# Kernel tuning notes

Measured on AMD Instinct MI355X. Metric: run time of the kernel, lower is better.

Reference implementation:

```python
import jax, jax.numpy as jnp
import numpy as np

B, T, K = 512, 1024, 64


def setup_inputs() -> dict:
    key = jax.random.key(0)
    k1, k2, k3, k4, k5 = jax.random.split(key, 5)
    emissions = jax.random.normal(k1, (B, T, K), dtype=jnp.float32)
    tags = jax.random.randint(k2, (B, T), 0, K, dtype=jnp.int64)
    mask = jnp.ones((B, T), dtype=bool)
    transitions = jax.random.uniform(k3, (K, K), minval=-0.1, maxval=0.1, dtype=jnp.float32)
    start_transitions = jax.random.uniform(k4, (K,), minval=-0.1, maxval=0.1, dtype=jnp.float32)
    end_transitions = jax.random.uniform(k5, (K,), minval=-0.1, maxval=0.1, dtype=jnp.float32)
    return {
        "emissions": emissions,
        "transitions": transitions,
        "start_transitions": start_transitions,
        "end_transitions": end_transitions,
        "tags": tags,
        "mask": mask,
    }


def _compute_score(emissions, transitions, start_transitions, end_transitions, tags, mask):
    # emissions: (B,T,K), tags: (B,T), mask: (B,T) bool
    maskf = mask.astype(emissions.dtype)
    # emission scores at gold tags, all positions: (B,T)
    emit = jnp.take_along_axis(emissions, tags[:, :, None], axis=2)[:, :, 0]
    score = emit[:, 0] + start_transitions[tags[:, 0]]
    # transition scores between consecutive gold tags: (B,T-1)
    trans = transitions[tags[:, :-1], tags[:, 1:]]
    score = score + jnp.sum((emit[:, 1:] + trans) * maskf[:, 1:], axis=1)
    seq_lengths = jnp.sum(mask.astype(jnp.int32), axis=1) - 1  # (B,)
    last_tags = jnp.take_along_axis(tags, seq_lengths[:, None], axis=1)[:, 0]
    score = score + end_transitions[last_tags]
    return score


def _log_partition(emissions, transitions, start_transitions, end_transitions, mask):
    maskf = mask.astype(emissions.dtype)
    alpha0 = emissions[:, 0] + start_transitions[None, :]  # (B,K)

    def step(alpha, xs):
        emit_t, mask_t = xs  # (B,K), (B,)
        # inner: (B, K_prev, K_cur)
        inner = alpha[:, :, None] + transitions[None, :, :] + emit_t[:, None, :]
        new_alpha = jax.nn.logsumexp(inner, axis=1)
        m = mask_t[:, None]
        alpha = new_alpha * m + alpha * (1.0 - m)
        return alpha, None

    xs = (jnp.swapaxes(emissions[:, 1:], 0, 1), jnp.swapaxes(maskf[:, 1:], 0, 1))
    alpha, _ = jax.lax.scan(step, alpha0, xs)
    alpha = alpha + end_transitions[None, :]
    return jax.nn.logsumexp(alpha, axis=1)  # (B,)


def reference(emissions, transitions, start_transitions, end_transitions, tags, mask):
    numerator = _compute_score(emissions, transitions, start_transitions, end_transitions, tags, mask)
    denominator = _log_partition(emissions, transitions, start_transitions, end_transitions, mask)
    return jnp.mean(denominator - numerator)
```

## Files before the change

### kernel.cpp

```cpp
#include <hip/hip_runtime.h>


#define CRF_B 512
#define CRF_T 1024
#define CRF_K 64

typedef float f32x2 __attribute__((ext_vector_type(2)));

#define SWZF(v, imm) \
  __int_as_float(__builtin_amdgcn_ds_swizzle(__float_as_int(v), (imm)))

#define DPPF(v, ctrl)                                                      \
  __int_as_float(__builtin_amdgcn_mov_dpp(__float_as_int(v), (ctrl), 0xF,  \
                                          0xF, true))
#define CTL_X1 0xB1
#define CTL_X2 0x4E
#define CTL_X3 0x1B
#define CTL_MIR 0x140
#define CTL_HMIR 0x141

__device__ __forceinline__ float red_add16(float x) {
  auto r = __builtin_amdgcn_permlane16_swap(__float_as_int(x),
                                            __float_as_int(x), false, false);
  return __int_as_float(r[0]) + __int_as_float(r[1]);
}
__device__ __forceinline__ float red_add32(float x) {
  auto r = __builtin_amdgcn_permlane32_swap(__float_as_int(x),
                                            __float_as_int(x), false, false);
  return __int_as_float(r[0]) + __int_as_float(r[1]);
}

#define SP2(x) ((f32x2){(x), (x)})
#define PFMA(b, k, acc) __builtin_elementwise_fma(SP2(b), (k), (acc))

#define PIN_P()                                                            \
  asm volatile("" : "+v"(kp0), "+v"(kp1), "+v"(kp2), "+v"(kp3), "+v"(kp4), \
                    "+v"(kp5), "+v"(kp6), "+v"(kp7), "+v"(kp8), "+v"(kp9), \
                    "+v"(kp10), "+v"(kp11), "+v"(kp12), "+v"(kp13),        \
                    "+v"(kp14), "+v"(kp15))
#define PIN_R()                                                            \
  asm volatile("" : "+v"(kr0), "+v"(kr1), "+v"(kr2), "+v"(kr3), "+v"(kr4), \
                    "+v"(kr5), "+v"(kr6), "+v"(kr7), "+v"(kr8), "+v"(kr9), \
                    "+v"(kr10), "+v"(kr11), "+v"(kr12), "+v"(kr13),        \
                    "+v"(kr14), "+v"(kr15))

#define GLOAD4(buf, ptr)                                                   \
  asm volatile("global_load_dword %0, %4, off\n\t"                         \
               "global_load_dword %1, %4, off offset:256\n\t"              \
               "global_load_dword %2, %4, off offset:512\n\t"              \
               "global_load_dword %3, %4, off offset:768"                  \
               : "=v"(buf[0]), "=v"(buf[1]), "=v"(buf[2]), "=v"(buf[3])    \
               : "v"(ptr))

#define WAITN(n)                                                           \
  do {                                                                     \
    asm volatile("s_waitcnt vmcnt(" #n ")" ::: "memory");                  \
    __builtin_amdgcn_sched_barrier(0);                                     \
  } while (0)

#define STEP(EV, APPLY, DOMAX)                                             \
  do {                                                                     \
    float t1 = DPPF(sv, CTL_X1), t2 = DPPF(sv, CTL_X2);                    \
    float t3 = DPPF(sv, CTL_X3);                                           \
    float t7 = DPPF(sv, CTL_HMIR), tF = DPPF(sv, CTL_MIR);                 \
    float t4 = DPPF(t7, CTL_X3), t5 = DPPF(t7, CTL_X2);                    \
    float t6 = DPPF(t7, CTL_X1), t8 = DPPF(t7, CTL_MIR);                   \
    float tC = DPPF(tF, CTL_X3), tD = DPPF(tF, CTL_X2);                    \
    float tE = DPPF(tF, CTL_X1);                                           \
    float t9 = DPPF(t8, CTL_X1), tA = DPPF(t8, CTL_X2);                    \
    float tB = DPPF(t8, CTL_X3);                                           \
    float xe = __expf(EV);                                                 \
    if (APPLY) xe = ldexpf(xe, -exs);                                      \
    f32x2 accP = SP2(sv) * kp0, accR = SP2(sv) * kr0;                      \
    f32x2 accQ = SP2(t1) * kp1, accS = SP2(t1) * kr1;                      \
    accP = PFMA(t2, kp2, accP);   accR = PFMA(t2, kr2, accR);              \
    accQ = PFMA(t3, kp3, accQ);   accS = PFMA(t3, kr3, accS);              \
    accP = PFMA(t4, kp4, accP);   accR = PFMA(t4, kr4, accR);              \
    accQ = PFMA(t5, kp5, accQ);   accS = PFMA(t5, kr5, accS);              \
    accP = PFMA(t6, kp6, accP);   accR = PFMA(t6, kr6, accR);              \
    accQ = PFMA(t7, kp7, accQ);   accS = PFMA(t7, kr7, accS);              \
    accP = PFMA(t8, kp8, accP);   accR = PFMA(t8, kr8, accR);              \
    accQ = PFMA(t9, kp9, accQ);   accS = PFMA(t9, kr9, accS);              \
    accP = PFMA(tA, kp10, accP);  accR = PFMA(tA, kr10, accR);             \
    accQ = PFMA(tB, kp11, accQ);  accS = PFMA(tB, kr11, accS);             \
    accP = PFMA(tC, kp12, accP);  accR = PFMA(tC, kr12, accR);             \
    accQ = PFMA(tD, kp13, accQ);  accS = PFMA(tD, kr13, accS);             \
    accP = PFMA(tE, kp14, accP);  accR = PFMA(tE, kr14, accR);             \
    accQ = PFMA(tF, kp15, accQ);  accS = PFMA(tF, kr15, accS);             \
    f32x2 a01 = accP + accQ;                                               \
    f32x2 a23 = accR + accS;                                               \
    auto eA = __builtin_amdgcn_permlane32_swap(                            \
        __float_as_int(a01.x), __float_as_int(a23.x), false, false);       \
    float sE = __int_as_float(eA[0]) + __int_as_float(eA[1]);              \
    auto oA = __builtin_amdgcn_permlane32_swap(                            \
        __float_as_int(a01.y), __float_as_int(a23.y), false, false);       \
    float sO = __int_as_float(oA[0]) + __int_as_float(oA[1]);              \
    auto fB = __builtin_amdgcn_permlane16_swap(                            \
        __float_as_int(sE), __float_as_int(sO), false, false);             \
    float red = __int_as_float(fB[0]) + __int_as_float(fB[1]);             \
    sv = red * xe;                                                         \
    if (DOMAX) {                                                           \
      int exl;                                                             \
      (void)frexpf(sv, &exl);                                              \
      exs = __builtin_amdgcn_readfirstlane(exl);                           \
      cexp += exs;                                                         \
    }                                                                      \
  } while (0)

__global__ void __attribute__((amdgpu_flat_work_group_size(64, 64)))
__attribute__((amdgpu_waves_per_eu(1, 1))) crf_fused_kernel(
    const float* __restrict__ emissions, const float* __restrict__ transitions,
    const float* __restrict__ start_t, const float* __restrict__ end_t,
    const int* __restrict__ tags32, float* __restrict__ d_out) {
  const int l = threadIdx.x;
  const int q = l >> 4;
  const int r = l & 15;
  const int b = blockIdx.x;

  f32x2 kp0, kp1, kp2, kp3, kp4, kp5, kp6, kp7;
  f32x2 kp8, kp9, kp10, kp11, kp12, kp13, kp14, kp15;
  f32x2 kr0, kr1, kr2, kr3, kr4, kr5, kr6, kr7;
  f32x2 kr8, kr9, kr10, kr11, kr12, kr13, kr14, kr15;
#define LK(pv, rv, m)                                                  \
  do {                                                                 \
    const float* row = transitions + (16 * q + (r ^ (m))) * CRF_K + r; \
    pv = (f32x2){__expf(row[0]), __expf(row[16])};                     \
    rv = (f32x2){__expf(row[32]), __expf(row[48])};                    \
  } while (0)
  LK(kp0, kr0, 0);   LK(kp1, kr1, 1);   LK(kp2, kr2, 2);
  LK(kp3, kr3, 3);   LK(kp4, kr4, 4);   LK(kp5, kr5, 5);
  LK(kp6, kr6, 6);   LK(kp7, kr7, 7);   LK(kp8, kr8, 8);
  LK(kp9, kr9, 9);   LK(kp10, kr10, 10); LK(kp11, kr11, 11);
  LK(kp12, kr12, 12); LK(kp13, kr13, 13); LK(kp14, kr14, 14);
  LK(kp15, kr15, 15);
#undef LK
  PIN_P();
  PIN_R();

  const float* eptr = emissions + (size_t)b * (CRF_T * CRF_K) + l;

  float sv = __expf(eptr[0] + start_t[l]);
  int exs, cexp = 0;
  {
    int exl;
    (void)frexpf(sv, &exl);
    exs = __builtin_amdgcn_readfirstlane(exl);
    cexp += exs;
  }

  float ea[4], eb[4], ec[4];
  const float* p = eptr + CRF_K;
  GLOAD4(ea, p);
  p += 4 * CRF_K;
  GLOAD4(eb, p);
  p += 4 * CRF_K;

  for (int gg = 0; gg < 84; ++gg) {
    PIN_P();
    PIN_R();
    GLOAD4(ec, p);
    p += 4 * CRF_K;
    WAITN(8);
    STEP(ea[0], true, false);
    STEP(ea[1], false, false);
    STEP(ea[2], false, false);
    STEP(ea[3], false, true);
    GLOAD4(ea, p);
    p += 4 * CRF_K;
    WAITN(8);
    STEP(eb[0], true, false);
    STEP(eb[1], false, false);
    STEP(eb[2], false, false);
    STEP(eb[3], false, true);
    GLOAD4(eb, p);
    p += 4 * CRF_K;
    WAITN(8);
    STEP(ec[0], true, false);
    STEP(ec[1], false, false);
    STEP(ec[2], false, false);
    STEP(ec[3], false, true);
  }

  float ecl[4], eal[3];
#pragma unroll
  for (int k = 0; k < 4; ++k) ecl[k] = eptr[(size_t)(1017 + k) * CRF_K];
#pragma unroll
  for (int k = 0; k < 3; ++k) eal[k] = eptr[(size_t)(1021 + k) * CRF_K];
  WAITN(11);
  STEP(ea[0], true, false);
  STEP(ea[1], false, false);
  STEP(ea[2], false, false);
  STEP(ea[3], false, true);
  WAITN(7);
  STEP(eb[0], true, false);
  STEP(eb[1], false, false);
  STEP(eb[2], false, false);
  STEP(eb[3], false, true);
  STEP(ecl[0], true, false);
  STEP(ecl[1], false, false);
  STEP(ecl[2], false, false);
  STEP(ecl[3], false, true);
  STEP(eal[0], true, false);
  STEP(eal[1], false, false);
  STEP(eal[2], false, false);

  float v = sv * __expf(end_t[l]);
  v += SWZF(v, 0x041F);
  v += SWZF(v, 0x081F);
  v += SWZF(v, 0x101F);
  v += SWZF(v, 0x201F);
  v = red_add32(red_add16(v));
  const float logZ = (float)cexp * 0.69314718055994530942f + logf(v);

  int hv = tags32[2 * l + 1];
  unsigned long long any = __ballot(hv != 0);
  const int mult = (any == 0ULL) ? 2 : 1;
  const size_t tbase = (size_t)b * CRF_T;
  const float* ebase = emissions + (size_t)b * (CRF_T * CRF_K);

  float sacc = 0.f;
#pragma unroll
  for (int it = 0; it < 16; ++it) {
    const int t = l + 64 * it;
    const int tg = tags32[(tbase + (size_t)t) * (size_t)mult];
    float c = ebase[(size_t)t * CRF_K + tg];
    if (t == 0)
      c += start_t[tg];
    else
      c += transitions[tags32[(tbase + (size_t)t - 1) * (size_t)mult] * CRF_K +
                       tg];
    if (t == CRF_T - 1) c += end_t[tg];
    sacc += c;
  }
  sacc += SWZF(sacc, 0x041F);
  sacc += SWZF(sacc, 0x081F);
  sacc += SWZF(sacc, 0x101F);
  sacc += SWZF(sacc, 0x201F);
  sacc = red_add32(red_add16(sacc));

  if (l == 0) d_out[b] = logZ - sacc;
}

__global__ __launch_bounds__(512) void crf_final_kernel(
    const float* __restrict__ d, float* __restrict__ out) {
  const int tid = threadIdx.x;
  float v = d[tid];
#pragma unroll
  for (int off = 32; off >= 1; off >>= 1) v += __shfl_xor(v, off, 64);
  __shared__ float red[8];
  if ((tid & 63) == 0) red[tid >> 6] = v;
  __syncthreads();
  if (tid == 0) {
    float s = 0.f;
#pragma unroll
    for (int i = 0; i < 8; ++i) s += red[i];
    out[0] = s * (1.0f / CRF_B);
  }
}

extern "C" void kernel_launch(void* const* d_in, const int* in_sizes, int n_in,
                              void* d_out, int out_size, void* d_ws,
                              size_t ws_size, hipStream_t stream) {
  const float* emissions   = (const float*)d_in[0];
  const float* transitions = (const float*)d_in[1];
  const float* start_t     = (const float*)d_in[2];
  const float* end_t       = (const float*)d_in[3];
  const int*   tags        = (const int*)d_in[4];

  float* out = (float*)d_out;
  float* d   = (float*)d_ws;

  crf_fused_kernel<<<CRF_B, 64, 0, stream>>>(emissions, transitions, start_t,
                                             end_t, tags, d);
  crf_final_kernel<<<1, 512, 0, stream>>>(d, out);
}
```

Baseline: 303.4 us.

## Process two batch rows per wavefront with interleaved forward recurrences

Each 64-lane block now runs the forward recurrence for two sequences at once, interleaving two independent dependency chains so their latencies can hide each other. The grid is halved to 256 blocks, and the transition matrix held in registers is shared by both chains. The cost is more registers and emission loads per wave, and with only 256 blocks on a GPU that has more CUs than that, some CUs may sit idle. The serial chain per block also becomes longer.

```diff
diff --git a/kernel.cpp b/kernel.cpp
--- a/kernel.cpp
+++ b/kernel.cpp
@@ -58,7 +58,7 @@
     __builtin_amdgcn_sched_barrier(0);                                     \
   } while (0)
 
-#define STEP(EV, APPLY, DOMAX)                                             \
+#define STEPC(sv, exs, cexp, EV, APPLY, DOMAX)                             \
   do {                                                                     \
     float t1 = DPPF(sv, CTL_X1), t2 = DPPF(sv, CTL_X2);                    \
     float t3 = DPPF(sv, CTL_X3);                                           \
@@ -107,6 +107,12 @@
     }                                                                      \
   } while (0)
 
+#define STEP2(EVA, EVB, APPLY, DOMAX)                                      \
+  do {                                                                     \
+    STEPC(svA, exsA, cexpA, EVA, APPLY, DOMAX);                            \
+    STEPC(svB, exsB, cexpB, EVB, APPLY, DOMAX);                            \
+  } while (0)
+
 __global__ void __attribute__((amdgpu_flat_work_group_size(64, 64)))
 __attribute__((amdgpu_waves_per_eu(1, 1))) crf_fused_kernel(
     const float* __restrict__ emissions, const float* __restrict__ transitions,
@@ -115,7 +121,8 @@
   const int l = threadIdx.x;
   const int q = l >> 4;
   const int r = l & 15;
-  const int b = blockIdx.x;
+  const int b0 = 2 * blockIdx.x;
+  const int b1 = b0 + 1;
 
   f32x2 kp0, kp1, kp2, kp3, kp4, kp5, kp6, kp7;
   f32x2 kp8, kp9, kp10, kp11, kp12, kp13, kp14, kp15;
@@ -137,108 +144,150 @@
   PIN_P();
   PIN_R();
 
-  const float* eptr = emissions + (size_t)b * (CRF_T * CRF_K) + l;
-
-  float sv = __expf(eptr[0] + start_t[l]);
-  int exs, cexp = 0;
+  const float* eptrA = emissions + (size_t)b0 * (CRF_T * CRF_K) + l;
+  const float* eptrB = emissions + (size_t)b1 * (CRF_T * CRF_K) + l;
+
+  float svA = __expf(eptrA[0] + start_t[l]);
+  float svB = __expf(eptrB[0] + start_t[l]);
+  int exsA, exsB, cexpA = 0, cexpB = 0;
   {
     int exl;
-    (void)frexpf(sv, &exl);
-    exs = __builtin_amdgcn_readfirstlane(exl);
-    cexp += exs;
-  }
-
-  float ea[4], eb[4], ec[4];
-  const float* p = eptr + CRF_K;
-  GLOAD4(ea, p);
-  p += 4 * CRF_K;
-  GLOAD4(eb, p);
-  p += 4 * CRF_K;
+    (void)frexpf(svA, &exl);
+    exsA = __builtin_amdgcn_readfirstlane(exl);
+    cexpA += exsA;
+    (void)frexpf(svB, &exl);
+    exsB = __builtin_amdgcn_readfirstlane(exl);
+    cexpB += exsB;
+  }
+
+  float eaA[4], ebA[4], ecA[4], eaB[4], ebB[4], ecB[4];
+  const float* pA = eptrA + CRF_K;
+  const float* pB = eptrB + CRF_K;
+  GLOAD4(eaA, pA);
+  GLOAD4(eaB, pB);
+  pA += 4 * CRF_K;
+  pB += 4 * CRF_K;
+  GLOAD4(ebA, pA);
+  GLOAD4(ebB, pB);
+  pA += 4 * CRF_K;
+  pB += 4 * CRF_K;
 
   for (int gg = 0; gg < 84; ++gg) {
     PIN_P();
     PIN_R();
-    GLOAD4(ec, p);
-    p += 4 * CRF_K;
-    WAITN(8);
-    STEP(ea[0], true, false);
-    STEP(ea[1], false, false);
-    STEP(ea[2], false, false);
-    STEP(ea[3], false, true);
-    GLOAD4(ea, p);
-    p += 4 * CRF_K;
-    WAITN(8);
-    STEP(eb[0], true, false);
-    STEP(eb[1], false, false);
-    STEP(eb[2], false, false);
-    STEP(eb[3], false, true);
-    GLOAD4(eb, p);
-    p += 4 * CRF_K;
-    WAITN(8);
-    STEP(ec[0], true, false);
-    STEP(ec[1], false, false);
-    STEP(ec[2], false, false);
-    STEP(ec[3], false, true);
-  }
-
-  float ecl[4], eal[3];
-#pragma unroll
-  for (int k = 0; k < 4; ++k) ecl[k] = eptr[(size_t)(1017 + k) * CRF_K];
-#pragma unroll
-  for (int k = 0; k < 3; ++k) eal[k] = eptr[(size_t)(1021 + k) * CRF_K];
-  WAITN(11);
-  STEP(ea[0], true, false);
-  STEP(ea[1], false, false);
-  STEP(ea[2], false, false);
-  STEP(ea[3], false, true);
-  WAITN(7);
-  STEP(eb[0], true, false);
-  STEP(eb[1], false, false);
-  STEP(eb[2], false, false);
-  STEP(eb[3], false, true);
-  STEP(ecl[0], true, false);
-  STEP(ecl[1], false, false);
-  STEP(ecl[2], false, false);
-  STEP(ecl[3], false, true);
-  STEP(eal[0], true, false);
-  STEP(eal[1], false, false);
-  STEP(eal[2], false, false);
-
-  float v = sv * __expf(end_t[l]);
-  v += SWZF(v, 0x041F);
-  v += SWZF(v, 0x081F);
-  v += SWZF(v, 0x101F);
-  v += SWZF(v, 0x201F);
-  v = red_add32(red_add16(v));
-  const float logZ = (float)cexp * 0.69314718055994530942f + logf(v);
+    GLOAD4(ecA, pA);
+    GLOAD4(ecB, pB);
+    pA += 4 * CRF_K;
+    pB += 4 * CRF_K;
+    WAITN(16);
+    STEP2(eaA[0], eaB[0], true, false);
+    STEP2(eaA[1], eaB[1], false, false);
+    STEP2(eaA[2], eaB[2], false, false);
+    STEP2(eaA[3], eaB[3], false, true);
+    GLOAD4(eaA, pA);
+    GLOAD4(eaB, pB);
+    pA += 4 * CRF_K;
+    pB += 4 * CRF_K;
+    WAITN(16);
+    STEP2(ebA[0], ebB[0], true, false);
+    STEP2(ebA[1], ebB[1], false, false);
+    STEP2(ebA[2], ebB[2], false, false);
+    STEP2(ebA[3], ebB[3], false, true);
+    GLOAD4(ebA, pA);
+    GLOAD4(ebB, pB);
+    pA += 4 * CRF_K;
+    pB += 4 * CRF_K;
+    WAITN(16);
+    STEP2(ecA[0], ecB[0], true, false);
+    STEP2(ecA[1], ecB[1], false, false);
+    STEP2(ecA[2], ecB[2], false, false);
+    STEP2(ecA[3], ecB[3], false, true);
+  }
+
+  float eclA[4], ealA[3], eclB[4], ealB[3];
+#pragma unroll
+  for (int k = 0; k < 4; ++k) {
+    eclA[k] = eptrA[(size_t)(1017 + k) * CRF_K];
+    eclB[k] = eptrB[(size_t)(1017 + k) * CRF_K];
+  }
+#pragma unroll
+  for (int k = 0; k < 3; ++k) {
+    ealA[k] = eptrA[(size_t)(1021 + k) * CRF_K];
+    ealB[k] = eptrB[(size_t)(1021 + k) * CRF_K];
+  }
+  WAITN(0);
+  STEP2(eaA[0], eaB[0], true, false);
+  STEP2(eaA[1], eaB[1], false, false);
+  STEP2(eaA[2], eaB[2], false, false);
+  STEP2(eaA[3], eaB[3], false, true);
+  STEP2(ebA[0], ebB[0], true, false);
+  STEP2(ebA[1], ebB[1], false, false);
+  STEP2(ebA[2], ebB[2], false, false);
+  STEP2(ebA[3], ebB[3], false, true);
+  STEP2(eclA[0], eclB[0], true, false);
+  STEP2(eclA[1], eclB[1], false, false);
+  STEP2(eclA[2], eclB[2], false, false);
+  STEP2(eclA[3], eclB[3], false, true);
+  STEP2(ealA[0], ealB[0], true, false);
+  STEP2(ealA[1], ealB[1], false, false);
+  STEP2(ealA[2], ealB[2], false, false);
+
+  float ee = __expf(end_t[l]);
+  float logZA, logZB;
+  {
+    float v = svA * ee;
+    v += SWZF(v, 0x041F);
+    v += SWZF(v, 0x081F);
+    v += SWZF(v, 0x101F);
+    v += SWZF(v, 0x201F);
+    v = red_add32(red_add16(v));
+    logZA = (float)cexpA * 0.69314718055994530942f + logf(v);
+  }
+  {
+    float v = svB * ee;
+    v += SWZF(v, 0x041F);
+    v += SWZF(v, 0x081F);
+    v += SWZF(v, 0x101F);
+    v += SWZF(v, 0x201F);
+    v = red_add32(red_add16(v));
+    logZB = (float)cexpB * 0.69314718055994530942f + logf(v);
+  }
 
   int hv = tags32[2 * l + 1];
   unsigned long long any = __ballot(hv != 0);
   const int mult = (any == 0ULL) ? 2 : 1;
-  const size_t tbase = (size_t)b * CRF_T;
-  const float* ebase = emissions + (size_t)b * (CRF_T * CRF_K);
-
-  float sacc = 0.f;
-#pragma unroll
-  for (int it = 0; it < 16; ++it) {
-    const int t = l + 64 * it;
-    const int tg = tags32[(tbase + (size_t)t) * (size_t)mult];
-    float c = ebase[(size_t)t * CRF_K + tg];
-    if (t == 0)
-      c += start_t[tg];
-    else
-      c += transitions[tags32[(tbase + (size_t)t - 1) * (size_t)mult] * CRF_K +
-                       tg];
-    if (t == CRF_T - 1) c += end_t[tg];
-    sacc += c;
-  }
-  sacc += SWZF(sacc, 0x041F);
-  sacc += SWZF(sacc, 0x081F);
-  sacc += SWZF(sacc, 0x101F);
-  sacc += SWZF(sacc, 0x201F);
-  sacc = red_add32(red_add16(sacc));
-
-  if (l == 0) d_out[b] = logZ - sacc;
+
+  float sc[2];
+#pragma unroll
+  for (int c = 0; c < 2; ++c) {
+    const size_t tbase = (size_t)(b0 + c) * CRF_T;
+    const float* ebase = emissions + (size_t)(b0 + c) * (CRF_T * CRF_K);
+    float sacc = 0.f;
+#pragma unroll
+    for (int it = 0; it < 16; ++it) {
+      const int t = l + 64 * it;
+      const int tg = tags32[(tbase + (size_t)t) * (size_t)mult];
+      float cv = ebase[(size_t)t * CRF_K + tg];
+      if (t == 0)
+        cv += start_t[tg];
+      else
+        cv += transitions[tags32[(tbase + (size_t)t - 1) * (size_t)mult] *
+                              CRF_K + tg];
+      if (t == CRF_T - 1) cv += end_t[tg];
+      sacc += cv;
+    }
+    sacc += SWZF(sacc, 0x041F);
+    sacc += SWZF(sacc, 0x081F);
+    sacc += SWZF(sacc, 0x101F);
+    sacc += SWZF(sacc, 0x201F);
+    sacc = red_add32(red_add16(sacc));
+    sc[c] = sacc;
+  }
+
+  if (l == 0) {
+    d_out[b0] = logZA - sc[0];
+    d_out[b1] = logZB - sc[1];
+  }
 }
 
 __global__ __launch_bounds__(512) void crf_final_kernel(
@@ -270,7 +319,7 @@
   float* out = (float*)d_out;
   float* d   = (float*)d_ws;
 
-  crf_fused_kernel<<<CRF_B, 64, 0, stream>>>(emissions, transitions, start_t,
-                                             end_t, tags, d);
+  crf_fused_kernel<<<CRF_B / 2, 64, 0, stream>>>(emissions, transitions,
+                                                 start_t, end_t, tags, d);
   crf_final_kernel<<<1, 512, 0, stream>>>(d, out);
 }
```

New measurement: 437.4 us. 44.2% more time.

## Restructure CRF forward step to per-lane output with cross-row shuffles instead of permlane reductions

Applied to the files above, without the earlier changes.

Each lane now computes its full output column directly. Three xor-shuffles broadcast the other 16-lane row groups of alpha, DPP permutations run within each group, and a scalar FMA chain with register-resident exp(transitions) follows. This removes the packed f32x2 FMAs and the permlane32/16 swap reduction tree at the end of each step. The cost is 64 scalar FMAs per step instead of 32 packed ones, plus __shfl_xor calls, which may lower to ds_bpermute through LDS and add latency on the serial recurrence.

```diff
diff --git a/kernel.cpp b/kernel.cpp
--- a/kernel.cpp
+++ b/kernel.cpp
@@ -5,7 +5,7 @@
 #define CRF_T 1024
 #define CRF_K 64
 
-typedef float f32x2 __attribute__((ext_vector_type(2)));
+typedef float f32x4 __attribute__((ext_vector_type(4)));
 
 #define SWZF(v, imm) \
   __int_as_float(__builtin_amdgcn_ds_swizzle(__float_as_int(v), (imm)))
@@ -30,19 +30,11 @@
   return __int_as_float(r[0]) + __int_as_float(r[1]);
 }
 
-#define SP2(x) ((f32x2){(x), (x)})
-#define PFMA(b, k, acc) __builtin_elementwise_fma(SP2(b), (k), (acc))
-
-#define PIN_P()                                                            \
-  asm volatile("" : "+v"(kp0), "+v"(kp1), "+v"(kp2), "+v"(kp3), "+v"(kp4), \
-                    "+v"(kp5), "+v"(kp6), "+v"(kp7), "+v"(kp8), "+v"(kp9), \
-                    "+v"(kp10), "+v"(kp11), "+v"(kp12), "+v"(kp13),        \
-                    "+v"(kp14), "+v"(kp15))
-#define PIN_R()                                                            \
-  asm volatile("" : "+v"(kr0), "+v"(kr1), "+v"(kr2), "+v"(kr3), "+v"(kr4), \
-                    "+v"(kr5), "+v"(kr6), "+v"(kr7), "+v"(kr8), "+v"(kr9), \
-                    "+v"(kr10), "+v"(kr11), "+v"(kr12), "+v"(kr13),        \
-                    "+v"(kr14), "+v"(kr15))
+#define PIN_K()                                                            \
+  asm volatile("" : "+v"(k0_0), "+v"(k0_1), "+v"(k0_2), "+v"(k0_3),        \
+                    "+v"(k1_0), "+v"(k1_1), "+v"(k1_2), "+v"(k1_3),        \
+                    "+v"(k2_0), "+v"(k2_1), "+v"(k2_2), "+v"(k2_3),        \
+                    "+v"(k3_0), "+v"(k3_1), "+v"(k3_2), "+v"(k3_3))
 
 #define GLOAD4(buf, ptr)                                                   \
   asm volatile("global_load_dword %0, %4, off\n\t"                         \
@@ -58,46 +50,42 @@
     __builtin_amdgcn_sched_barrier(0);                                     \
   } while (0)
 
+#define GROUP(S, aE, aO, kv0, kv1, kv2, kv3)                               \
+  {                                                                        \
+    float t7 = DPPF(S, CTL_HMIR);                                          \
+    float tF = DPPF(S, CTL_MIR);                                           \
+    float t8 = DPPF(t7, CTL_MIR);                                          \
+    aE = (S)*kv0[0];                                                       \
+    aO = DPPF(S, CTL_X1) * kv0[1];                                         \
+    aE = fmaf(DPPF(S, CTL_X2), kv0[2], aE);                                \
+    aO = fmaf(DPPF(S, CTL_X3), kv0[3], aO);                                \
+    aE = fmaf(DPPF(t7, CTL_X3), kv1[0], aE);                               \
+    aO = fmaf(DPPF(t7, CTL_X2), kv1[1], aO);                               \
+    aE = fmaf(DPPF(t7, CTL_X1), kv1[2], aE);                               \
+    aO = fmaf(t7, kv1[3], aO);                                             \
+    aE = fmaf(t8, kv2[0], aE);                                             \
+    aO = fmaf(DPPF(t8, CTL_X1), kv2[1], aO);                               \
+    aE = fmaf(DPPF(t8, CTL_X2), kv2[2], aE);                               \
+    aO = fmaf(DPPF(t8, CTL_X3), kv2[3], aO);                               \
+    aE = fmaf(DPPF(tF, CTL_X3), kv3[0], aE);                               \
+    aO = fmaf(DPPF(tF, CTL_X2), kv3[1], aO);                               \
+    aE = fmaf(DPPF(tF, CTL_X1), kv3[2], aE);                               \
+    aO = fmaf(tF, kv3[3], aO);                                             \
+  }
+
 #define STEP(EV, APPLY, DOMAX)                                             \
   do {                                                                     \
-    float t1 = DPPF(sv, CTL_X1), t2 = DPPF(sv, CTL_X2);                    \
-    float t3 = DPPF(sv, CTL_X3);                                           \
-    float t7 = DPPF(sv, CTL_HMIR), tF = DPPF(sv, CTL_MIR);                 \
-    float t4 = DPPF(t7, CTL_X3), t5 = DPPF(t7, CTL_X2);                    \
-    float t6 = DPPF(t7, CTL_X1), t8 = DPPF(t7, CTL_MIR);                   \
-    float tC = DPPF(tF, CTL_X3), tD = DPPF(tF, CTL_X2);                    \
-    float tE = DPPF(tF, CTL_X1);                                           \
-    float t9 = DPPF(t8, CTL_X1), tA = DPPF(t8, CTL_X2);                    \
-    float tB = DPPF(t8, CTL_X3);                                           \
+    float s1 = __shfl_xor(sv, 16, 64);                                     \
+    float s2 = __shfl_xor(sv, 32, 64);                                     \
+    float s3 = __shfl_xor(sv, 48, 64);                                     \
     float xe = __expf(EV);                                                 \
     if (APPLY) xe = ldexpf(xe, -exs);                                      \
-    f32x2 accP = SP2(sv) * kp0, accR = SP2(sv) * kr0;                      \
-    f32x2 accQ = SP2(t1) * kp1, accS = SP2(t1) * kr1;                      \
-    accP = PFMA(t2, kp2, accP);   accR = PFMA(t2, kr2, accR);              \
-    accQ = PFMA(t3, kp3, accQ);   accS = PFMA(t3, kr3, accS);              \
-    accP = PFMA(t4, kp4, accP);   accR = PFMA(t4, kr4, accR);              \
-    accQ = PFMA(t5, kp5, accQ);   accS = PFMA(t5, kr5, accS);              \
-    accP = PFMA(t6, kp6, accP);   accR = PFMA(t6, kr6, accR);              \
-    accQ = PFMA(t7, kp7, accQ);   accS = PFMA(t7, kr7, accS);              \
-    accP = PFMA(t8, kp8, accP);   accR = PFMA(t8, kr8, accR);              \
-    accQ = PFMA(t9, kp9, accQ);   accS = PFMA(t9, kr9, accS);              \
-    accP = PFMA(tA, kp10, accP);  accR = PFMA(tA, kr10, accR);             \
-    accQ = PFMA(tB, kp11, accQ);  accS = PFMA(tB, kr11, accS);             \
-    accP = PFMA(tC, kp12, accP);  accR = PFMA(tC, kr12, accR);             \
-    accQ = PFMA(tD, kp13, accQ);  accS = PFMA(tD, kr13, accS);             \
-    accP = PFMA(tE, kp14, accP);  accR = PFMA(tE, kr14, accR);             \
-    accQ = PFMA(tF, kp15, accQ);  accS = PFMA(tF, kr15, accS);             \
-    f32x2 a01 = accP + accQ;                                               \
-    f32x2 a23 = accR + accS;                                               \
-    auto eA = __builtin_amdgcn_permlane32_swap(                            \
-        __float_as_int(a01.x), __float_as_int(a23.x), false, false);       \
-    float sE = __int_as_float(eA[0]) + __int_as_float(eA[1]);              \
-    auto oA = __builtin_amdgcn_permlane32_swap(                            \
-        __float_as_int(a01.y), __float_as_int(a23.y), false, false);       \
-    float sO = __int_as_float(oA[0]) + __int_as_float(oA[1]);              \
-    auto fB = __builtin_amdgcn_permlane16_swap(                            \
-        __float_as_int(sE), __float_as_int(sO), false, false);             \
-    float red = __int_as_float(fB[0]) + __int_as_float(fB[1]);             \
+    float aE0, aO0, aE1, aO1, aE2, aO2, aE3, aO3;                          \
+    GROUP(sv, aE0, aO0, k0_0, k0_1, k0_2, k0_3);                           \
+    GROUP(s1, aE1, aO1, k1_0, k1_1, k1_2, k1_3);                           \
+    GROUP(s2, aE2, aO2, k2_0, k2_1, k2_2, k2_3);                           \
+    GROUP(s3, aE3, aO3, k3_0, k3_1, k3_2, k3_3);                           \
+    float red = ((aE0 + aO0) + (aE1 + aO1)) + ((aE2 + aO2) + (aE3 + aO3)); \
     sv = red * xe;                                                         \
     if (DOMAX) {                                                           \
       int exl;                                                             \
@@ -113,29 +101,25 @@
     const float* __restrict__ start_t, const float* __restrict__ end_t,
     const int* __restrict__ tags32, float* __restrict__ d_out) {
   const int l = threadIdx.x;
-  const int q = l >> 4;
-  const int r = l & 15;
   const int b = blockIdx.x;
 
-  f32x2 kp0, kp1, kp2, kp3, kp4, kp5, kp6, kp7;
-  f32x2 kp8, kp9, kp10, kp11, kp12, kp13, kp14, kp15;
-  f32x2 kr0, kr1, kr2, kr3, kr4, kr5, kr6, kr7;
-  f32x2 kr8, kr9, kr10, kr11, kr12, kr13, kr14, kr15;
-#define LK(pv, rv, m)                                                  \
-  do {                                                                 \
-    const float* row = transitions + (16 * q + (r ^ (m))) * CRF_K + r; \
-    pv = (f32x2){__expf(row[0]), __expf(row[16])};                     \
-    rv = (f32x2){__expf(row[32]), __expf(row[48])};                    \
-  } while (0)
-  LK(kp0, kr0, 0);   LK(kp1, kr1, 1);   LK(kp2, kr2, 2);
-  LK(kp3, kr3, 3);   LK(kp4, kr4, 4);   LK(kp5, kr5, 5);
-  LK(kp6, kr6, 6);   LK(kp7, kr7, 7);   LK(kp8, kr8, 8);
-  LK(kp9, kr9, 9);   LK(kp10, kr10, 10); LK(kp11, kr11, 11);
-  LK(kp12, kr12, 12); LK(kp13, kr13, 13); LK(kp14, kr14, 14);
-  LK(kp15, kr15, 15);
-#undef LK
-  PIN_P();
-  PIN_R();
+  f32x4 k0_0, k0_1, k0_2, k0_3, k1_0, k1_1, k1_2, k1_3;
+  f32x4 k2_0, k2_1, k2_2, k2_3, k3_0, k3_1, k3_2, k3_3;
+#define LKG(kv, c, mb)                                                       \
+  kv = (f32x4){                                                              \
+      __expf(transitions[(size_t)((l ^ (mb)) ^ (16 * (c))) * CRF_K + l]),    \
+      __expf(transitions[(size_t)((l ^ ((mb) + 1)) ^ (16 * (c))) * CRF_K +   \
+                         l]),                                                \
+      __expf(transitions[(size_t)((l ^ ((mb) + 2)) ^ (16 * (c))) * CRF_K +   \
+                         l]),                                                \
+      __expf(transitions[(size_t)((l ^ ((mb) + 3)) ^ (16 * (c))) * CRF_K +   \
+                         l])}
+  LKG(k0_0, 0, 0);  LKG(k0_1, 0, 4);  LKG(k0_2, 0, 8);  LKG(k0_3, 0, 12);
+  LKG(k1_0, 1, 0);  LKG(k1_1, 1, 4);  LKG(k1_2, 1, 8);  LKG(k1_3, 1, 12);
+  LKG(k2_0, 2, 0);  LKG(k2_1, 2, 4);  LKG(k2_2, 2, 8);  LKG(k2_3, 2, 12);
+  LKG(k3_0, 3, 0);  LKG(k3_1, 3, 4);  LKG(k3_2, 3, 8);  LKG(k3_3, 3, 12);
+#undef LKG
+  PIN_K();
 
   const float* eptr = emissions + (size_t)b * (CRF_T * CRF_K) + l;
 
@@ -156,8 +140,7 @@
   p += 4 * CRF_K;
 
   for (int gg = 0; gg < 84; ++gg) {
-    PIN_P();
-    PIN_R();
+    PIN_K();
     GLOAD4(ec, p);
     p += 4 * CRF_K;
     WAITN(8);
```

Measured after the change: 413.5 us. +36.3%, slower.
